# Optimization experiments

Measured on AMD Instinct MI355X. Metric: run time of the kernel, lower is better.

The kernel has to match this reference:

```python
import jax, jax.numpy as jnp
import numpy as np

KERNEL = 3          # kernel_size = (3, 3)
DEGREE = 3          # spline_order -> Chebyshev polynomial degree
N_CONVS = 8


def setup_inputs() -> dict:
    key = jax.random.key(0)
    k1, k2, k3, k4 = jax.random.split(key, 4)
    x = jax.random.normal(k1, (16, 16, 128, 128), jnp.float32)
    # per-conv learned params of ChebyshevKANLinear(in=9, out=1), stacked over n_convs
    cheby_coeffs = jax.random.normal(k2, (N_CONVS, KERNEL * KERNEL, DEGREE + 1), jnp.float32) * 0.1
    base_weight = jax.random.normal(k3, (N_CONVS, KERNEL * KERNEL), jnp.float32) * (1.0 / 3.0)
    spline_scaler = 1.0 + 0.1 * jax.random.normal(k4, (N_CONVS, KERNEL * KERNEL), jnp.float32)
    return {"x": x, "cheby_coeffs": cheby_coeffs,
            "base_weight": base_weight, "spline_scaler": spline_scaler}


def _kan_conv2d(x, cheby_coeffs, base_weight, spline_scaler):
    # x: (B, C, H, W); each channel unfolded independently (as torch Unfold per-channel),
    # each of N_CONVS KAN kernels applied to every channel -> out channels C*N_CONVS.
    B, C, H, W = x.shape
    patches = jax.lax.conv_general_dilated_patches(
        x, (KERNEL, KERNEL), (1, 1), [(1, 1), (1, 1)])  # (B, C*9, Ho, Wo), channel-major
    Ho, Wo = patches.shape[-2], patches.shape[-1]
    p = patches.reshape(B, C, KERNEL * KERNEL, Ho * Wo)
    p = jnp.moveaxis(p, 2, 3)  # (B, C, P, 9) where P = Ho*Wo patches

    # base (skip) path: SiLU(x) @ base_weight^T
    base = jnp.einsum('bcpi,ji->bcjp', jax.nn.silu(p), base_weight)

    # spline path: Chebyshev basis on tanh-normalized input
    t = jnp.tanh(p)
    Ts = [jnp.ones_like(t), t]
    for _ in range(DEGREE - 1):
        Ts.append(2.0 * t * Ts[-1] - Ts[-2])
    Tb = jnp.stack(Ts, axis=-1)  # (B, C, P, 9, DEGREE+1)
    w = cheby_coeffs * spline_scaler[..., None]  # (n_convs, 9, D+1)
    spline = jnp.einsum('bcpik,jik->bcjp', Tb, w)

    out = (base + spline).reshape(B, C * N_CONVS, Ho, Wo)
    return out


def reference(x, cheby_coeffs, base_weight, spline_scaler):
    return _kan_conv2d(x, cheby_coeffs, base_weight, spline_scaler)
```

## Files before the change

kernel.cpp:

```cpp
#include <hip/hip_runtime.h>

#define BATCH 16
#define CH    16
#define HH    128
#define WW    128
#define NC    8
#define TS    32
#define HALO  (TS + 2)

__global__ __launch_bounds__(256, 4)
void kan_conv_kernel(const float* __restrict__ x,
                     const float* __restrict__ cheby,
                     const float* __restrict__ bwt,
                     const float* __restrict__ scl,
                     float* __restrict__ out)
{
    __shared__ float4 feat[HALO][HALO];
    __shared__ float4 wgt[9 * NC];
    __shared__ float  bias[NC];

    const int tx  = threadIdx.x;
    const int ty  = threadIdx.y;
    const int tid = ty * 32 + tx;

    const int w0 = blockIdx.x * TS;
    const int h0 = blockIdx.y * TS;
    const int bz = blockIdx.z;

    if (tid < 9 * NC) {
        int j = tid / 9, i = tid % 9;
        float s  = scl[j * 9 + i];
        float w1 = cheby[(j * 9 + i) * 4 + 1] * s;
        float w2 = cheby[(j * 9 + i) * 4 + 2] * s;
        float w3 = cheby[(j * 9 + i) * 4 + 3] * s;
        wgt[i * NC + j] = make_float4(bwt[j * 9 + i], w1, w2, w3);
    } else if (tid >= 128 && tid < 128 + NC) {
        int j = tid - 128;
        float b = 0.f;
        #pragma unroll
        for (int i = 0; i < 9; ++i)
            b += (cheby[(j * 9 + i) * 4 + 0] - cheby[(j * 9 + i) * 4 + 2]) * scl[j * 9 + i];
        bias[j] = b;
    }

    const float* xp = x + (size_t)bz * HH * WW;
    for (int idx = tid; idx < HALO * HALO; idx += 256) {
        int r  = idx / HALO;
        int c  = idx - r * HALO;
        int gh = h0 + r - 1;
        int gw = w0 + c - 1;
        float v = 0.f;
        if ((unsigned)gh < (unsigned)HH && (unsigned)gw < (unsigned)WW)
            v = xp[gh * WW + gw];
        float e2 = __expf(2.f * v);
        float t  = 1.f - 2.f * __builtin_amdgcn_rcpf(e2 + 1.f);
        float sg = __builtin_amdgcn_rcpf(1.f + __expf(-v));
        float f0 = v * sg;
        float f2 = 2.f * t * t;
        float f3 = 2.f * t * (f2 - 1.f) - t;
        feat[r][c] = make_float4(f0, t, f2, f3);
    }
    __syncthreads();

    float acc[4][NC];
    #pragma unroll
    for (int p = 0; p < 4; ++p)
        #pragma unroll
        for (int j = 0; j < NC; ++j)
            acc[p][j] = bias[j];

    #pragma unroll 1
    for (int i = 0; i < 9; ++i) {
        const int dr = i / 3, dc = i - 3 * (i / 3);
        float4 w[NC];
        #pragma unroll
        for (int j = 0; j < NC; ++j) w[j] = wgt[i * NC + j];
        #pragma unroll
        for (int p = 0; p < 4; ++p) {
            float4 f = feat[ty * 4 + p + dr][tx + dc];
            #pragma unroll
            for (int j = 0; j < NC; ++j) {
                acc[p][j] += w[j].x * f.x;
                acc[p][j] += w[j].y * f.y;
                acc[p][j] += w[j].z * f.z;
                acc[p][j] += w[j].w * f.w;
            }
        }
    }

    #pragma unroll
    for (int p = 0; p < 4; ++p) {
        const int gh = h0 + ty * 4 + p;
        float* op = out + ((size_t)(bz * NC) * HH + gh) * WW + w0 + tx;
        #pragma unroll
        for (int j = 0; j < NC; ++j)
            op[(size_t)j * HH * WW] = acc[p][j];
    }
}

extern "C" void kernel_launch(void* const* d_in, const int* in_sizes, int n_in,
                              void* d_out, int out_size, void* d_ws, size_t ws_size,
                              hipStream_t stream) {
    const float* x     = (const float*)d_in[0];
    const float* cheby = (const float*)d_in[1];
    const float* bwt   = (const float*)d_in[2];
    const float* scl   = (const float*)d_in[3];
    float* out = (float*)d_out;

    dim3 grid(WW / TS, HH / TS, BATCH * CH);
    dim3 block(32, 8);
    hipLaunchKernelGGL(kan_conv_kernel, grid, block, 0, stream, x, cheby, bwt, scl, out);
}
```

Before: 174.0 us.

## Tile by full-width row bands with vectorized loads and 8 rows per thread

Result: slower. 265.9 us (+52.7%).

```diff
diff --git a/kernel.cpp b/kernel.cpp
--- a/kernel.cpp
+++ b/kernel.cpp
@@ -5,8 +5,9 @@
 #define HH    128
 #define WW    128
 #define NC    8
-#define TS    32
-#define HALO  (TS + 2)
+#define TR    16
+#define HR    (TR + 2)
+#define FW    (WW + 2)
 
 __global__ __launch_bounds__(256, 4)
 void kan_conv_kernel(const float* __restrict__ x,
@@ -15,17 +16,13 @@
                      const float* __restrict__ scl,
                      float* __restrict__ out)
 {
-    __shared__ float4 feat[HALO][HALO];
+    __shared__ float4 feat[HR][FW];
     __shared__ float4 wgt[9 * NC];
     __shared__ float  bias[NC];
 
-    const int tx  = threadIdx.x;
-    const int ty  = threadIdx.y;
-    const int tid = ty * 32 + tx;
-
-    const int w0 = blockIdx.x * TS;
-    const int h0 = blockIdx.y * TS;
-    const int bz = blockIdx.z;
+    const int tid  = threadIdx.x;
+    const int band = blockIdx.x * TR;
+    const int bz   = blockIdx.y;
 
     if (tid < 9 * NC) {
         int j = tid / 9, i = tid % 9;
@@ -44,58 +41,68 @@
     }
 
     const float* xp = x + (size_t)bz * HH * WW;
-    for (int idx = tid; idx < HALO * HALO; idx += 256) {
-        int r  = idx / HALO;
-        int c  = idx - r * HALO;
-        int gh = h0 + r - 1;
-        int gw = w0 + c - 1;
-        float v = 0.f;
-        if ((unsigned)gh < (unsigned)HH && (unsigned)gw < (unsigned)WW)
-            v = xp[gh * WW + gw];
-        float e2 = __expf(2.f * v);
-        float t  = 1.f - 2.f * __builtin_amdgcn_rcpf(e2 + 1.f);
-        float sg = __builtin_amdgcn_rcpf(1.f + __expf(-v));
-        float f0 = v * sg;
-        float f2 = 2.f * t * t;
-        float f3 = 2.f * t * (f2 - 1.f) - t;
-        feat[r][c] = make_float4(f0, t, f2, f3);
+    for (int idx = tid; idx < HR * (WW / 4); idx += 256) {
+        int row = idx >> 5;
+        int cg  = idx & 31;
+        int gh  = band + row - 1;
+        float4 v = make_float4(0.f, 0.f, 0.f, 0.f);
+        if ((unsigned)gh < (unsigned)HH)
+            v = ((const float4*)(xp + gh * WW))[cg];
+        float vv[4] = {v.x, v.y, v.z, v.w};
+        #pragma unroll
+        for (int k = 0; k < 4; ++k) {
+            float val = vv[k];
+            float e1 = __expf(val);
+            float e2 = __expf(2.f * val);
+            float sg = 1.f - __builtin_amdgcn_rcpf(1.f + e1);
+            float t  = 1.f - 2.f * __builtin_amdgcn_rcpf(e2 + 1.f);
+            float f2 = 2.f * t * t;
+            float f3 = 2.f * t * (f2 - 1.f) - t;
+            feat[row][1 + cg * 4 + k] = make_float4(val * sg, t, f2, f3);
+        }
+    }
+    if (tid < HR) {
+        feat[tid][0]      = make_float4(0.f, 0.f, 0.f, 0.f);
+        feat[tid][FW - 1] = make_float4(0.f, 0.f, 0.f, 0.f);
     }
     __syncthreads();
 
-    float acc[4][NC];
+    const int c  = tid & 127;
+    const int r0 = tid >> 7;
+
+    float acc[8][NC];
     #pragma unroll
-    for (int p = 0; p < 4; ++p)
+    for (int s = 0; s < 8; ++s)
         #pragma unroll
         for (int j = 0; j < NC; ++j)
-            acc[p][j] = bias[j];
+            acc[s][j] = bias[j];
 
-    #pragma unroll 1
+    #pragma unroll
     for (int i = 0; i < 9; ++i) {
-        const int dr = i / 3, dc = i - 3 * (i / 3);
-        float4 w[NC];
+        const int dr = i / 3, dc = i % 3;
+        float4 f[8];
         #pragma unroll
-        for (int j = 0; j < NC; ++j) w[j] = wgt[i * NC + j];
+        for (int s = 0; s < 8; ++s)
+            f[s] = feat[r0 + 2 * s + dr][c + dc];
         #pragma unroll
-        for (int p = 0; p < 4; ++p) {
-            float4 f = feat[ty * 4 + p + dr][tx + dc];
+        for (int j = 0; j < NC; ++j) {
+            float4 w = wgt[i * NC + j];
             #pragma unroll
-            for (int j = 0; j < NC; ++j) {
-                acc[p][j] += w[j].x * f.x;
-                acc[p][j] += w[j].y * f.y;
-                acc[p][j] += w[j].z * f.z;
-                acc[p][j] += w[j].w * f.w;
+            for (int s = 0; s < 8; ++s) {
+                acc[s][j] += w.x * f[s].x;
+                acc[s][j] += w.y * f[s].y;
+                acc[s][j] += w.z * f[s].z;
+                acc[s][j] += w.w * f[s].w;
             }
         }
     }
 
+    float* op = out + (size_t)(bz * NC) * HH * WW + (band + r0) * WW + c;
     #pragma unroll
-    for (int p = 0; p < 4; ++p) {
-        const int gh = h0 + ty * 4 + p;
-        float* op = out + ((size_t)(bz * NC) * HH + gh) * WW + w0 + tx;
+    for (int j = 0; j < NC; ++j)
         #pragma unroll
-        for (int j = 0; j < NC; ++j)
-            op[(size_t)j * HH * WW] = acc[p][j];
-    }
+        for (int s = 0; s < 8; ++s)
+            op[(size_t)j * HH * WW + s * 2 * WW] = acc[s][j];
 }
 
 extern "C" void kernel_launch(void* const* d_in, const int* in_sizes, int n_in,
@@ -107,7 +114,7 @@
     const float* scl   = (const float*)d_in[3];
     float* out = (float*)d_out;
 
-    dim3 grid(WW / TS, HH / TS, BATCH * CH);
-    dim3 block(32, 8);
+    dim3 grid(HH / TR, BATCH * CH);
+    dim3 block(256);
     hipLaunchKernelGGL(kan_conv_kernel, grid, block, 0, stream, x, cheby, bwt, scl, out);
 }
```
